# Kernel optimization log

Hardware: AMD Instinct MI355X
Metric: run time of the kernel (lower is better)

Reference implementation:

```python
import jax, jax.numpy as jnp
import numpy as np

T, N, F_IN = 5, 10000, 16
E = 160000
C = 32          # gat_hidden_dim (per head)
H0 = 2          # heads in layer 0 (concat) -> out 64
GRU = 64
OUT_H = 32


def setup_inputs() -> dict:
    key = jax.random.key(0)
    ks = jax.random.split(key, 24)
    s = 0.1
    inp = {
        "x_seq": jax.random.normal(ks[0], (T, N, F_IN), jnp.float32),
        "edge_index": jax.random.randint(ks[1], (2, E), 0, N, jnp.int32),
        # GAT layer 0: in 16 -> 2 heads x 32, concat -> 64
        "gat0_W": s * jax.random.normal(ks[2], (F_IN, H0 * C), jnp.float32),
        "gat0_asrc": s * jax.random.normal(ks[3], (H0, C), jnp.float32),
        "gat0_adst": s * jax.random.normal(ks[4], (H0, C), jnp.float32),
        "gat0_b": s * jax.random.normal(ks[5], (H0 * C,), jnp.float32),
        "res0_W": s * jax.random.normal(ks[6], (F_IN, H0 * C), jnp.float32),   # [in,out]
        # GAT layer 1: in 64 -> 1 head x 32, no concat -> 32
        "gat1_W": s * jax.random.normal(ks[7], (H0 * C, C), jnp.float32),
        "gat1_asrc": s * jax.random.normal(ks[8], (1, C), jnp.float32),
        "gat1_adst": s * jax.random.normal(ks[9], (1, C), jnp.float32),
        "gat1_b": s * jax.random.normal(ks[10], (C,), jnp.float32),
        "res1_W": s * jax.random.normal(ks[11], (H0 * C, C), jnp.float32),
        # GRU cells (torch GRUCell layout: W_i [3H,in], W_h [3H,H])
        "gru0_Wi": s * jax.random.normal(ks[12], (3 * GRU, C), jnp.float32),
        "gru0_Wh": s * jax.random.normal(ks[13], (3 * GRU, GRU), jnp.float32),
        "gru0_bi": s * jax.random.normal(ks[14], (3 * GRU,), jnp.float32),
        "gru0_bh": s * jax.random.normal(ks[15], (3 * GRU,), jnp.float32),
        "gru1_Wi": s * jax.random.normal(ks[16], (3 * GRU, GRU), jnp.float32),
        "gru1_Wh": s * jax.random.normal(ks[17], (3 * GRU, GRU), jnp.float32),
        "gru1_bi": s * jax.random.normal(ks[18], (3 * GRU,), jnp.float32),
        "gru1_bh": s * jax.random.normal(ks[19], (3 * GRU,), jnp.float32),
        # MLP head
        "fc1_W": s * jax.random.normal(ks[20], (GRU, OUT_H), jnp.float32),
        "fc1_b": s * jax.random.normal(ks[21], (OUT_H,), jnp.float32),
        "fc2_W": s * jax.random.normal(ks[22], (OUT_H, 1), jnp.float32),
        "fc2_b": s * jax.random.normal(ks[23], (1,), jnp.float32),
    }
    return inp


def _gat(x, src, dst, n, W, a_src, a_dst, b, heads, concat):
    ch = W.shape[1] // heads
    xw = (x @ W).reshape(n, heads, ch)                      # [N,H,C]
    al_s = (xw * a_src).sum(-1)                             # [N,H]
    al_d = (xw * a_dst).sum(-1)
    e = jax.nn.leaky_relu(al_s[src] + al_d[dst], 0.2)       # [Etot,H]
    m = jax.ops.segment_max(e, dst, num_segments=n)
    ex = jnp.exp(e - m[dst])
    den = jax.ops.segment_sum(ex, dst, num_segments=n)
    alpha = ex / (den[dst] + 1e-16)                         # scatter-softmax
    out = jax.ops.segment_sum(alpha[:, :, None] * xw[src], dst, num_segments=n)
    out = out.reshape(n, heads * ch) if concat else out.mean(axis=1)
    return out + b


def _gru(x, h, Wi, Wh, bi, bh):
    gi = x @ Wi.T + bi
    gh = h @ Wh.T + bh
    i_r, i_z, i_n = jnp.split(gi, 3, axis=-1)
    h_r, h_z, h_n = jnp.split(gh, 3, axis=-1)
    r = jax.nn.sigmoid(i_r + h_r)
    z = jax.nn.sigmoid(i_z + h_z)
    nn_ = jnp.tanh(i_n + r * h_n)
    return (1.0 - z) * nn_ + z * h


def reference(x_seq, edge_index,
              gat0_W, gat0_asrc, gat0_adst, gat0_b, res0_W,
              gat1_W, gat1_asrc, gat1_adst, gat1_b, res1_W,
              gru0_Wi, gru0_Wh, gru0_bi, gru0_bh,
              gru1_Wi, gru1_Wh, gru1_bi, gru1_bh,
              fc1_W, fc1_b, fc2_W, fc2_b):
    n = x_seq.shape[1]
    loops = jnp.arange(n, dtype=edge_index.dtype)
    src = jnp.concatenate([edge_index[0], loops])           # PyG adds self-loops
    dst = jnp.concatenate([edge_index[1], loops])

    def step(carry, x_t):
        h0, h1 = carry
        x1 = jax.nn.elu(_gat(x_t, src, dst, n, gat0_W, gat0_asrc, gat0_adst, gat0_b, 2, True)) + x_t @ res0_W
        x2 = jax.nn.elu(_gat(x1, src, dst, n, gat1_W, gat1_asrc, gat1_adst, gat1_b, 1, False)) + x1 @ res1_W
        h0 = _gru(x2, h0, gru0_Wi, gru0_Wh, gru0_bi, gru0_bh)
        h1 = _gru(h0, h1, gru1_Wi, gru1_Wh, gru1_bi, gru1_bh)
        return (h0, h1), None

    h0 = jnp.zeros((n, gru0_Wh.shape[1]), x_seq.dtype)
    h1 = jnp.zeros((n, gru1_Wh.shape[1]), x_seq.dtype)
    (h0, h1), _ = jax.lax.scan(step, (h0, h1), x_seq)
    h = jax.nn.relu(h1 @ fc1_W + fc1_b)
    return h @ fc2_W + fc2_b                                # [N,1]
```

## Files before the change

kernel.cpp:

```cpp
#include <hip/hip_runtime.h>
#include <hip/hip_bf16.h>
#include <math.h>

#define T_STEPS 5
#define NNODES  10000
#define NM      (T_STEPS * NNODES)
#define F_IN    16
#define NEDGES  160000
#define ETOT    (NEDGES + NNODES)

__global__ __launch_bounds__(256) void k_count(const int* __restrict__ ei, int* __restrict__ counts) {
    int idx = blockIdx.x * 256 + threadIdx.x;
    if (idx >= ETOT) return;
    int dst = (idx < NEDGES) ? ei[NEDGES + idx] : (idx - NEDGES);
    atomicAdd(&counts[dst], 1);
}

__global__ __launch_bounds__(1024) void k_scan(const int* __restrict__ counts, int* __restrict__ offs) {
    __shared__ int ssum[1024];
    int t = threadIdx.x;
    const int chunk = (NNODES + 1023) / 1024;
    int start = t * chunk, end = min(start + chunk, NNODES);
    int s = 0;
    for (int i = start; i < end; i++) s += counts[i];
    ssum[t] = s;
    __syncthreads();
    for (int off = 1; off < 1024; off <<= 1) {
        int v = (t >= off) ? ssum[t - off] : 0;
        __syncthreads();
        ssum[t] += v;
        __syncthreads();
    }
    int excl = (t == 0) ? 0 : ssum[t - 1];
    for (int i = start; i < end; i++) { offs[i] = excl; excl += counts[i]; }
    if (t == 1023) offs[NNODES] = ssum[1023];
}

__global__ __launch_bounds__(256) void k_fill(const int* __restrict__ ei, const int* __restrict__ offs,
                                              int* __restrict__ cursor, int* __restrict__ csr) {
    int idx = blockIdx.x * 256 + threadIdx.x;
    if (idx >= ETOT) return;
    int src, dst;
    if (idx < NEDGES) { src = ei[idx]; dst = ei[NEDGES + idx]; }
    else              { src = dst = idx - NEDGES; }
    int p = atomicAdd(&cursor[dst], 1);
    csr[offs[dst] + p] = src;
}

__global__ __launch_bounds__(256) void k_transpose(const float* __restrict__ Wi0, const float* __restrict__ Wh0,
                                                   const float* __restrict__ Wi1, const float* __restrict__ Wh1,
                                                   float* __restrict__ WiT0, float* __restrict__ WhT0,
                                                   float* __restrict__ WiT1, float* __restrict__ WhT1) {
    int idx = blockIdx.x * 256 + threadIdx.x;
    if (idx < 32 * 192) {
        int k = idx / 192, r = idx % 192;
        WiT0[idx] = Wi0[r * 32 + k];
        return;
    }
    idx -= 32 * 192;
    if (idx < 64 * 192) {
        int k = idx / 192, r = idx % 192;
        WhT0[idx] = Wh0[r * 64 + k];
        return;
    }
    idx -= 64 * 192;
    if (idx < 64 * 192) {
        int k = idx / 192, r = idx % 192;
        WiT1[idx] = Wi1[r * 64 + k];
        return;
    }
    idx -= 64 * 192;
    if (idx < 64 * 192) {
        int k = idx / 192, r = idx % 192;
        WhT1[idx] = Wh1[r * 64 + k];
    }
}

__global__ __launch_bounds__(256) void k_mm0_all(const float* __restrict__ x,
                                                 const float* __restrict__ W,
                                                 const float* __restrict__ Wres,
                                                 const float* __restrict__ asrc,
                                                 const float* __restrict__ adst,
                                                 float* __restrict__ xw, float* __restrict__ xres,
                                                 float* __restrict__ als, float* __restrict__ ald) {
    int wave = threadIdx.x >> 6, lane = threadIdx.x & 63;
    int m = blockIdx.x * 4 + wave;
    if (m >= NM) return;
    const float* xr = x + (size_t)m * F_IN;
    float xreg[F_IN];
#pragma unroll
    for (int k = 0; k < F_IN; k++) xreg[k] = xr[k];
    float acc = 0.f, accr = 0.f;
#pragma unroll
    for (int k = 0; k < F_IN; k++) {
        acc  += xreg[k] * W[k * 64 + lane];
        accr += xreg[k] * Wres[k * 64 + lane];
    }
    xw[(size_t)m * 64 + lane]   = acc;
    xres[(size_t)m * 64 + lane] = accr;
    float ps = acc * asrc[lane], pd = acc * adst[lane];
    for (int off = 16; off; off >>= 1) {
        ps += __shfl_down(ps, off, 32);
        pd += __shfl_down(pd, off, 32);
    }
    if ((lane & 31) == 0) {
        int h = lane >> 5;
        als[m * 2 + h] = ps;
        ald[m * 2 + h] = pd;
    }
}

__global__ __launch_bounds__(256) void k_gat0_all(const float* __restrict__ xw,
                                                  const float* __restrict__ xres,
                                                  const float* __restrict__ als,
                                                  const float* __restrict__ ald,
                                                  const int* __restrict__ offs, const int* __restrict__ csr,
                                                  const float* __restrict__ b,
                                                  const float* __restrict__ W1,
                                                  const float* __restrict__ Wres1,
                                                  const float* __restrict__ as1,
                                                  const float* __restrict__ ad1v,
                                                  float* __restrict__ xw1, float* __restrict__ xres1,
                                                  float* __restrict__ als1, float* __restrict__ ald1) {
    int wave = threadIdx.x >> 6, lane = threadIdx.x & 63;
    int m = blockIdx.x * 4 + wave;
    if (m >= NM) return;
    int t = m / NNODES;
    int node = m - t * NNODES;
    int base = t * NNODES;
    int beg = offs[node], end = offs[node + 1];
    int deg = end - beg;
    float ad0 = ald[m * 2 + 0], ad1 = ald[m * 2 + 1];
    float acc;
    if (deg <= 64) {
        int s = 0; float e0 = -INFINITY, e1 = -INFINITY;
        if (lane < deg) {
            s = base + csr[beg + lane];
            e0 = als[s * 2 + 0] + ad0; e0 = e0 > 0.f ? e0 : 0.2f * e0;
            e1 = als[s * 2 + 1] + ad1; e1 = e1 > 0.f ? e1 : 0.2f * e1;
        }
        float m0 = e0, m1 = e1;
        for (int o = 32; o; o >>= 1) {
            m0 = fmaxf(m0, __shfl_xor(m0, o));
            m1 = fmaxf(m1, __shfl_xor(m1, o));
        }
        float ex0 = (lane < deg) ? expf(e0 - m0) : 0.f;
        float ex1 = (lane < deg) ? expf(e1 - m1) : 0.f;
        float d0 = ex0, d1 = ex1;
        for (int o = 32; o; o >>= 1) {
            d0 += __shfl_xor(d0, o);
            d1 += __shfl_xor(d1, o);
        }
        ex0 *= 1.f / (d0 + 1e-16f);
        ex1 *= 1.f / (d1 + 1e-16f);
        float a0 = 0.f, a1 = 0.f, a2 = 0.f, a3 = 0.f;
        int i = 0;
        for (; i + 4 <= deg; i += 4) {
            int   s0 = __shfl(s, i),     s1 = __shfl(s, i + 1), s2 = __shfl(s, i + 2), s3 = __shfl(s, i + 3);
            float u0 = __shfl(ex0, i),   v0 = __shfl(ex1, i);
            float u1 = __shfl(ex0, i+1), v1 = __shfl(ex1, i+1);
            float u2 = __shfl(ex0, i+2), v2 = __shfl(ex1, i+2);
            float u3 = __shfl(ex0, i+3), v3 = __shfl(ex1, i+3);
            a0 += (lane < 32 ? u0 : v0) * xw[(size_t)s0 * 64 + lane];
            a1 += (lane < 32 ? u1 : v1) * xw[(size_t)s1 * 64 + lane];
            a2 += (lane < 32 ? u2 : v2) * xw[(size_t)s2 * 64 + lane];
            a3 += (lane < 32 ? u3 : v3) * xw[(size_t)s3 * 64 + lane];
        }
        for (; i < deg; i++) {
            int s0 = __shfl(s, i);
            float u = __shfl(ex0, i), v = __shfl(ex1, i);
            a0 += (lane < 32 ? u : v) * xw[(size_t)s0 * 64 + lane];
        }
        acc = (a0 + a1) + (a2 + a3);
    } else {
        float m0 = -INFINITY, m1 = -INFINITY;
        for (int i = beg + lane; i < end; i += 64) {
            int s = base + csr[i];
            float e0 = als[s * 2 + 0] + ad0; e0 = e0 > 0.f ? e0 : 0.2f * e0;
            float e1 = als[s * 2 + 1] + ad1; e1 = e1 > 0.f ? e1 : 0.2f * e1;
            m0 = fmaxf(m0, e0); m1 = fmaxf(m1, e1);
        }
        for (int o = 32; o; o >>= 1) {
            m0 = fmaxf(m0, __shfl_xor(m0, o));
            m1 = fmaxf(m1, __shfl_xor(m1, o));
        }
        float d0 = 0.f, d1 = 0.f;
        for (int i = beg + lane; i < end; i += 64) {
            int s = base + csr[i];
            float e0 = als[s * 2 + 0] + ad0; e0 = e0 > 0.f ? e0 : 0.2f * e0;
            float e1 = als[s * 2 + 1] + ad1; e1 = e1 > 0.f ? e1 : 0.2f * e1;
            d0 += expf(e0 - m0); d1 += expf(e1 - m1);
        }
        for (int o = 32; o; o >>= 1) { d0 += __shfl_xor(d0, o); d1 += __shfl_xor(d1, o); }
        float inv0 = 1.f / (d0 + 1e-16f), inv1 = 1.f / (d1 + 1e-16f);
        acc = 0.f;
        for (int i = beg; i < end; i++) {
            int s = base + csr[i];
            float e, wgt;
            if (lane < 32) { e = als[s * 2 + 0] + ad0; e = e > 0.f ? e : 0.2f * e; wgt = expf(e - m0) * inv0; }
            else           { e = als[s * 2 + 1] + ad1; e = e > 0.f ? e : 0.2f * e; wgt = expf(e - m1) * inv1; }
            acc += wgt * xw[(size_t)s * 64 + lane];
        }
    }
    float x1v = acc + b[lane];
    x1v = x1v > 0.f ? x1v : expm1f(x1v);
    x1v += xres[(size_t)m * 64 + lane];
    int j = lane & 31;
    const float* Wp = (lane < 32) ? W1 : Wres1;
    float pacc = 0.f;
#pragma unroll
    for (int k = 0; k < 64; k++) {
        float xv = __shfl(x1v, k);
        pacc += xv * Wp[k * 32 + j];
    }
    if (lane < 32) xw1[(size_t)m * 32 + j]   = pacc;
    else           xres1[(size_t)m * 32 + j] = pacc;
    float ps = (lane < 32) ? pacc * as1[j]  : 0.f;
    float pd = (lane < 32) ? pacc * ad1v[j] : 0.f;
    for (int o = 16; o; o >>= 1) {
        ps += __shfl_down(ps, o, 32);
        pd += __shfl_down(pd, o, 32);
    }
    if (lane == 0) { als1[m] = ps; ald1[m] = pd; }
}

__global__ __launch_bounds__(256) void k_gat1_all(const float* __restrict__ xw1,
                                                  const float* __restrict__ xres1,
                                                  const float* __restrict__ als1,
                                                  const float* __restrict__ ald1,
                                                  const int* __restrict__ offs, const int* __restrict__ csr,
                                                  const float* __restrict__ b,
                                                  float* __restrict__ x2) {
    int wave = threadIdx.x >> 6, lane = threadIdx.x & 63;
    int m = blockIdx.x * 4 + wave;
    if (m >= NM) return;
    int t = m / NNODES;
    int node = m - t * NNODES;
    int base = t * NNODES;
    int beg = offs[node], end = offs[node + 1];
    int deg = end - beg;
    float adv = ald1[m];
    int ch = lane & 31, half = lane >> 5;
    float aggr;
    if (deg <= 64) {
        int s = 0; float e = -INFINITY;
        if (lane < deg) {
            s = base + csr[beg + lane];
            e = als1[s] + adv; e = e > 0.f ? e : 0.2f * e;
        }
        float mx = e;
        for (int o = 32; o; o >>= 1) mx = fmaxf(mx, __shfl_xor(mx, o));
        float ex = (lane < deg) ? expf(e - mx) : 0.f;
        float d = ex;
        for (int o = 32; o; o >>= 1) d += __shfl_xor(d, o);
        ex *= 1.f / (d + 1e-16f);
        float acc = 0.f;
        for (int i = 0; i < deg; i += 2) {
            int i2 = (i + 1 < deg) ? i + 1 : i;
            int   sa = __shfl(s, i),  sb = __shfl(s, i2);
            float wa = __shfl(ex, i), wb = __shfl(ex, i2);
            if (i + 1 >= deg) wb = 0.f;
            int   sm = half ? sb : sa;
            float wm = half ? wb : wa;
            acc += wm * xw1[(size_t)sm * 32 + ch];
        }
        acc += __shfl_xor(acc, 32);
        aggr = acc;
    } else {
        float mx = -INFINITY;
        for (int i = beg + lane; i < end; i += 64) {
            float e = als1[base + csr[i]] + adv; e = e > 0.f ? e : 0.2f * e;
            mx = fmaxf(mx, e);
        }
        for (int o = 32; o; o >>= 1) mx = fmaxf(mx, __shfl_xor(mx, o));
        float d = 0.f;
        for (int i = beg + lane; i < end; i += 64) {
            float e = als1[base + csr[i]] + adv; e = e > 0.f ? e : 0.2f * e;
            d += expf(e - mx);
        }
        for (int o = 32; o; o >>= 1) d += __shfl_xor(d, o);
        float inv = 1.f / (d + 1e-16f);
        float acc = 0.f;
        for (int i = beg; i < end; i++) {
            int s = base + csr[i];
            float e = als1[s] + adv; e = e > 0.f ? e : 0.2f * e;
            float wgt = expf(e - mx) * inv;
            acc += wgt * xw1[(size_t)s * 32 + ch];
        }
        aggr = acc;
    }
    if (lane < 32) {
        float v = aggr + b[ch];
        v = v > 0.f ? v : expm1f(v);
        x2[(size_t)m * 32 + ch] = v + xres1[(size_t)m * 32 + ch];
    }
}

__global__ __launch_bounds__(256) void k_gruhead(const float* __restrict__ x2,
                                                 const float* __restrict__ WiT0,
                                                 const float* __restrict__ WhT0,
                                                 const float* __restrict__ WiT1,
                                                 const float* __restrict__ WhT1,
                                                 const float* __restrict__ bi0, const float* __restrict__ bh0,
                                                 const float* __restrict__ bi1, const float* __restrict__ bh1,
                                                 const float* __restrict__ fc1W,
                                                 const float* __restrict__ fc1b,
                                                 const float* __restrict__ fc2W,
                                                 const float* __restrict__ fc2b,
                                                 float* __restrict__ out) {
    int wave = threadIdx.x >> 6, lane = threadIdx.x & 63;
    int node0 = (blockIdx.x * 4 + wave) * 2;

    float bir0 = bi0[lane], biz0 = bi0[64 + lane], bin0 = bi0[128 + lane];
    float bhr0 = bh0[lane], bhz0 = bh0[64 + lane], bhn0 = bh0[128 + lane];
    float bir1 = bi1[lane], biz1 = bi1[64 + lane], bin1 = bi1[128 + lane];
    float bhr1 = bh1[lane], bhz1 = bh1[64 + lane], bhn1 = bh1[128 + lane];

    float h0v0 = 0.f, h0v1 = 0.f, h1v0 = 0.f, h1v1 = 0.f;

    for (int t = 0; t < T_STEPS; t++) {
        float x2v = x2[((size_t)t * NNODES + node0) * 32 + lane];

        float gr0 = bir0, gz0 = biz0, gn0 = bin0, gr1 = bir0, gz1 = biz0, gn1 = bin0;
        float hr0 = bhr0, hz0 = bhz0, hn0 = bhn0, hr1 = bhr0, hz1 = bhz0, hn1 = bhn0;
#pragma unroll 8
        for (int k = 0; k < 32; k++) {
            float wr = WiT0[k * 192 + lane];
            float wz = WiT0[k * 192 + 64 + lane];
            float wn = WiT0[k * 192 + 128 + lane];
            float xa = __shfl(x2v, k);
            float xb = __shfl(x2v, 32 + k);
            gr0 += xa * wr; gz0 += xa * wz; gn0 += xa * wn;
            gr1 += xb * wr; gz1 += xb * wz; gn1 += xb * wn;
        }
#pragma unroll 8
        for (int k = 0; k < 64; k++) {
            float wr = WhT0[k * 192 + lane];
            float wz = WhT0[k * 192 + 64 + lane];
            float wn = WhT0[k * 192 + 128 + lane];
            float ha = __shfl(h0v0, k);
            float hb = __shfl(h0v1, k);
            hr0 += ha * wr; hz0 += ha * wz; hn0 += ha * wn;
            hr1 += hb * wr; hz1 += hb * wz; hn1 += hb * wn;
        }
        {
            float r0 = 1.f / (1.f + expf(-(gr0 + hr0)));
            float z0 = 1.f / (1.f + expf(-(gz0 + hz0)));
            float n0 = tanhf(gn0 + r0 * hn0);
            h0v0 = (1.f - z0) * n0 + z0 * h0v0;
            float r1 = 1.f / (1.f + expf(-(gr1 + hr1)));
            float z1 = 1.f / (1.f + expf(-(gz1 + hz1)));
            float n1 = tanhf(gn1 + r1 * hn1);
            h0v1 = (1.f - z1) * n1 + z1 * h0v1;
        }
        gr0 = bir1; gz0 = biz1; gn0 = bin1; gr1 = bir1; gz1 = biz1; gn1 = bin1;
        hr0 = bhr1; hz0 = bhz1; hn0 = bhn1; hr1 = bhr1; hz1 = bhz1; hn1 = bhn1;
#pragma unroll 4
        for (int k = 0; k < 64; k++) {
            float wir = WiT1[k * 192 + lane];
            float wiz = WiT1[k * 192 + 64 + lane];
            float win = WiT1[k * 192 + 128 + lane];
            float xa = __shfl(h0v0, k);
            float xb = __shfl(h0v1, k);
            gr0 += xa * wir; gz0 += xa * wiz; gn0 += xa * win;
            gr1 += xb * wir; gz1 += xb * wiz; gn1 += xb * win;
            float whr = WhT1[k * 192 + lane];
            float whz = WhT1[k * 192 + 64 + lane];
            float whn = WhT1[k * 192 + 128 + lane];
            float ha = __shfl(h1v0, k);
            float hb = __shfl(h1v1, k);
            hr0 += ha * whr; hz0 += ha * whz; hn0 += ha * whn;
            hr1 += hb * whr; hz1 += hb * whz; hn1 += hb * whn;
        }
        {
            float r0 = 1.f / (1.f + expf(-(gr0 + hr0)));
            float z0 = 1.f / (1.f + expf(-(gz0 + hz0)));
            float n0 = tanhf(gn0 + r0 * hn0);
            h1v0 = (1.f - z0) * n0 + z0 * h1v0;
            float r1 = 1.f / (1.f + expf(-(gr1 + hr1)));
            float z1 = 1.f / (1.f + expf(-(gz1 + hz1)));
            float n1 = tanhf(gn1 + r1 * hn1);
            h1v1 = (1.f - z1) * n1 + z1 * h1v1;
        }
    }

    int j = lane & 31, half = lane >> 5;
    float a = fc1b[j];
#pragma unroll
    for (int k = 0; k < 64; k++) {
        float h_a = __shfl(h1v0, k);
        float h_b = __shfl(h1v1, k);
        a += (half ? h_b : h_a) * fc1W[k * 32 + j];
    }
    a = fmaxf(a, 0.f);
    float v = a * fc2W[j];
    for (int o = 16; o; o >>= 1) v += __shfl_down(v, o, 32);
    if ((lane & 31) == 0) out[node0 + half] = v + fc2b[0];
}

extern "C" void kernel_launch(void* const* d_in, const int* in_sizes, int n_in,
                              void* d_out, int out_size, void* d_ws, size_t ws_size,
                              hipStream_t stream) {
    const float* x_seq   = (const float*)d_in[0];
    const int*   ei      = (const int*)d_in[1];
    const float* gat0_W  = (const float*)d_in[2];
    const float* gat0_as = (const float*)d_in[3];
    const float* gat0_ad = (const float*)d_in[4];
    const float* gat0_b  = (const float*)d_in[5];
    const float* res0_W  = (const float*)d_in[6];
    const float* gat1_W  = (const float*)d_in[7];
    const float* gat1_as = (const float*)d_in[8];
    const float* gat1_ad = (const float*)d_in[9];
    const float* gat1_b  = (const float*)d_in[10];
    const float* res1_W  = (const float*)d_in[11];
    const float* gru0_Wi = (const float*)d_in[12];
    const float* gru0_Wh = (const float*)d_in[13];
    const float* gru0_bi = (const float*)d_in[14];
    const float* gru0_bh = (const float*)d_in[15];
    const float* gru1_Wi = (const float*)d_in[16];
    const float* gru1_Wh = (const float*)d_in[17];
    const float* gru1_bi = (const float*)d_in[18];
    const float* gru1_bh = (const float*)d_in[19];
    const float* fc1_W   = (const float*)d_in[20];
    const float* fc1_b   = (const float*)d_in[21];
    const float* fc2_W   = (const float*)d_in[22];
    const float* fc2_b   = (const float*)d_in[23];
    float* out = (float*)d_out;

    char* w = (char*)d_ws;
    size_t off = 0;
    auto take = [&](size_t bytes) { size_t r = off; off += (bytes + 255) & ~(size_t)255; return r; };
    const size_t N = NNODES, M = NM;
    int*   counts = (int*)(w + take(N * 4));
    int*   cursor = (int*)(w + take(N * 4));
    int*   offs   = (int*)(w + take((N + 1) * 4));
    int*   csr    = (int*)(w + take((size_t)ETOT * 4));
    float* xw0    = (float*)(w + take(M * 64 * 4));
    float* xres0  = (float*)(w + take(M * 64 * 4));
    float* als0   = (float*)(w + take(M * 2 * 4));
    float* ald0   = (float*)(w + take(M * 2 * 4));
    float* xw1    = (float*)(w + take(M * 32 * 4));
    float* xres1  = (float*)(w + take(M * 32 * 4));
    float* als1   = (float*)(w + take(M * 4));
    float* ald1   = (float*)(w + take(M * 4));
    float* x2     = (float*)(w + take(M * 32 * 4));
    float* wiT0   = (float*)(w + take(32 * 192 * 4));
    float* whT0   = (float*)(w + take(64 * 192 * 4));
    float* wiT1   = (float*)(w + take(64 * 192 * 4));
    float* whT1   = (float*)(w + take(64 * 192 * 4));

    hipMemsetAsync(counts, 0, N * 4, stream);
    hipMemsetAsync(cursor, 0, N * 4, stream);
    const int egrid = (ETOT + 255) / 256;
    k_count<<<egrid, 256, 0, stream>>>(ei, counts);
    k_scan<<<1, 1024, 0, stream>>>(counts, offs);
    k_fill<<<egrid, 256, 0, stream>>>(ei, offs, cursor, csr);
    const int ttot = 32 * 192 + 3 * 64 * 192;
    k_transpose<<<(ttot + 255) / 256, 256, 0, stream>>>(gru0_Wi, gru0_Wh, gru1_Wi, gru1_Wh,
                                                        wiT0, whT0, wiT1, whT1);

    const int mgrid = (NM + 3) / 4;
    k_mm0_all<<<mgrid, 256, 0, stream>>>(x_seq, gat0_W, res0_W, gat0_as, gat0_ad, xw0, xres0, als0, ald0);
    k_gat0_all<<<mgrid, 256, 0, stream>>>(xw0, xres0, als0, ald0, offs, csr, gat0_b,
                                          gat1_W, res1_W, gat1_as, gat1_ad,
                                          xw1, xres1, als1, ald1);
    k_gat1_all<<<mgrid, 256, 0, stream>>>(xw1, xres1, als1, ald1, offs, csr, gat1_b, x2);

    const int ggrid = NNODES / 8;
    k_gruhead<<<ggrid, 256, 0, stream>>>(x2, wiT0, whT0, wiT1, whT1,
                                         gru0_bi, gru0_bh, gru1_bi, gru1_bh,
                                         fc1_W, fc1_b, fc2_W, fc2_b, out);
}
```

Before: 444.9 us.

## Process four nodes per wave in GRU head and use readlane broadcasts

The GRU/MLP head kernel now handles four nodes per wavefront instead of two, so each weight load is reused across more nodes. The r and z gate biases are pre-summed and the input and hidden matmuls are merged into shared accumulators. Lane broadcasts switch from __shfl (LDS-based permute) to the readlane builtin, which returns a wave-uniform scalar, and this also applies in the gat0 projection. The trade-offs are higher register pressure and half as many waves in the GRU kernel, which lowers occupancy.

```diff
diff --git a/kernel.cpp b/kernel.cpp
--- a/kernel.cpp
+++ b/kernel.cpp
@@ -8,6 +8,9 @@
 #define F_IN    16
 #define NEDGES  160000
 #define ETOT    (NEDGES + NNODES)
+#define GNPW    4
+
+#define RL(v, k) __int_as_float(__builtin_amdgcn_readlane(__float_as_int(v), (k)))
 
 __global__ __launch_bounds__(256) void k_count(const int* __restrict__ ei, int* __restrict__ counts) {
     int idx = blockIdx.x * 256 + threadIdx.x;
@@ -210,7 +213,7 @@
     float pacc = 0.f;
 #pragma unroll
     for (int k = 0; k < 64; k++) {
-        float xv = __shfl(x1v, k);
+        float xv = RL(x1v, k);
         pacc += xv * Wp[k * 32 + j];
     }
     if (lane < 32) xw1[(size_t)m * 32 + j]   = pacc;
@@ -309,93 +312,101 @@
                                                  const float* __restrict__ fc2b,
                                                  float* __restrict__ out) {
     int wave = threadIdx.x >> 6, lane = threadIdx.x & 63;
-    int node0 = (blockIdx.x * 4 + wave) * 2;
-
-    float bir0 = bi0[lane], biz0 = bi0[64 + lane], bin0 = bi0[128 + lane];
-    float bhr0 = bh0[lane], bhz0 = bh0[64 + lane], bhn0 = bh0[128 + lane];
-    float bir1 = bi1[lane], biz1 = bi1[64 + lane], bin1 = bi1[128 + lane];
-    float bhr1 = bh1[lane], bhz1 = bh1[64 + lane], bhn1 = bh1[128 + lane];
-
-    float h0v0 = 0.f, h0v1 = 0.f, h1v0 = 0.f, h1v1 = 0.f;
+    int node0 = (blockIdx.x * 4 + wave) * GNPW;
+
+    float bir0 = bi0[lane] + bh0[lane];
+    float biz0 = bi0[64 + lane] + bh0[64 + lane];
+    float bin0 = bi0[128 + lane], bhn0 = bh0[128 + lane];
+    float bir1 = bi1[lane] + bh1[lane];
+    float biz1 = bi1[64 + lane] + bh1[64 + lane];
+    float bin1 = bi1[128 + lane], bhn1 = bh1[128 + lane];
+
+    float h0[GNPW] = {0.f, 0.f, 0.f, 0.f};
+    float h1[GNPW] = {0.f, 0.f, 0.f, 0.f};
 
     for (int t = 0; t < T_STEPS; t++) {
-        float x2v = x2[((size_t)t * NNODES + node0) * 32 + lane];
-
-        float gr0 = bir0, gz0 = biz0, gn0 = bin0, gr1 = bir0, gz1 = biz0, gn1 = bin0;
-        float hr0 = bhr0, hz0 = bhz0, hn0 = bhn0, hr1 = bhr0, hz1 = bhz0, hn1 = bhn0;
+        float xa = x2[((size_t)t * NNODES + node0) * 32 + lane];
+        float xb = x2[((size_t)t * NNODES + node0) * 32 + 64 + lane];
+
+        float gr[GNPW], gz[GNPW], gin[GNPW], ghn[GNPW];
+#pragma unroll
+        for (int n = 0; n < GNPW; n++) { gr[n] = bir0; gz[n] = biz0; gin[n] = bin0; ghn[n] = bhn0; }
 #pragma unroll 8
         for (int k = 0; k < 32; k++) {
             float wr = WiT0[k * 192 + lane];
             float wz = WiT0[k * 192 + 64 + lane];
             float wn = WiT0[k * 192 + 128 + lane];
-            float xa = __shfl(x2v, k);
-            float xb = __shfl(x2v, 32 + k);
-            gr0 += xa * wr; gz0 += xa * wz; gn0 += xa * wn;
-            gr1 += xb * wr; gz1 += xb * wz; gn1 += xb * wn;
-        }
-#pragma unroll 8
+            float xv[GNPW];
+            xv[0] = RL(xa, k); xv[1] = RL(xa, 32 + k);
+            xv[2] = RL(xb, k); xv[3] = RL(xb, 32 + k);
+#pragma unroll
+            for (int n = 0; n < GNPW; n++) {
+                gr[n] += xv[n] * wr; gz[n] += xv[n] * wz; gin[n] += xv[n] * wn;
+            }
+        }
+#pragma unroll 4
         for (int k = 0; k < 64; k++) {
             float wr = WhT0[k * 192 + lane];
             float wz = WhT0[k * 192 + 64 + lane];
             float wn = WhT0[k * 192 + 128 + lane];
-            float ha = __shfl(h0v0, k);
-            float hb = __shfl(h0v1, k);
-            hr0 += ha * wr; hz0 += ha * wz; hn0 += ha * wn;
-            hr1 += hb * wr; hz1 += hb * wz; hn1 += hb * wn;
-        }
-        {
-            float r0 = 1.f / (1.f + expf(-(gr0 + hr0)));
-            float z0 = 1.f / (1.f + expf(-(gz0 + hz0)));
-            float n0 = tanhf(gn0 + r0 * hn0);
-            h0v0 = (1.f - z0) * n0 + z0 * h0v0;
-            float r1 = 1.f / (1.f + expf(-(gr1 + hr1)));
-            float z1 = 1.f / (1.f + expf(-(gz1 + hz1)));
-            float n1 = tanhf(gn1 + r1 * hn1);
-            h0v1 = (1.f - z1) * n1 + z1 * h0v1;
-        }
-        gr0 = bir1; gz0 = biz1; gn0 = bin1; gr1 = bir1; gz1 = biz1; gn1 = bin1;
-        hr0 = bhr1; hz0 = bhz1; hn0 = bhn1; hr1 = bhr1; hz1 = bhz1; hn1 = bhn1;
+#pragma unroll
+            for (int n = 0; n < GNPW; n++) {
+                float hv = RL(h0[n], k);
+                gr[n] += hv * wr; gz[n] += hv * wz; ghn[n] += hv * wn;
+            }
+        }
+#pragma unroll
+        for (int n = 0; n < GNPW; n++) {
+            float r = 1.f / (1.f + expf(-gr[n]));
+            float z = 1.f / (1.f + expf(-gz[n]));
+            float nn = tanhf(gin[n] + r * ghn[n]);
+            h0[n] = (1.f - z) * nn + z * h0[n];
+        }
+
+#pragma unroll
+        for (int n = 0; n < GNPW; n++) { gr[n] = bir1; gz[n] = biz1; gin[n] = bin1; ghn[n] = bhn1; }
 #pragma unroll 4
         for (int k = 0; k < 64; k++) {
             float wir = WiT1[k * 192 + lane];
             float wiz = WiT1[k * 192 + 64 + lane];
             float win = WiT1[k * 192 + 128 + lane];
-            float xa = __shfl(h0v0, k);
-            float xb = __shfl(h0v1, k);
-            gr0 += xa * wir; gz0 += xa * wiz; gn0 += xa * win;
-            gr1 += xb * wir; gz1 += xb * wiz; gn1 += xb * win;
             float whr = WhT1[k * 192 + lane];
             float whz = WhT1[k * 192 + 64 + lane];
             float whn = WhT1[k * 192 + 128 + lane];
-            float ha = __shfl(h1v0, k);
-            float hb = __shfl(h1v1, k);
-            hr0 += ha * whr; hz0 += ha * whz; hn0 += ha * whn;
-            hr1 += hb * whr; hz1 += hb * whz; hn1 += hb * whn;
-        }
-        {
-            float r0 = 1.f / (1.f + expf(-(gr0 + hr0)));
-            float z0 = 1.f / (1.f + expf(-(gz0 + hz0)));
-            float n0 = tanhf(gn0 + r0 * hn0);
-            h1v0 = (1.f - z0) * n0 + z0 * h1v0;
-            float r1 = 1.f / (1.f + expf(-(gr1 + hr1)));
-            float z1 = 1.f / (1.f + expf(-(gz1 + hz1)));
-            float n1 = tanhf(gn1 + r1 * hn1);
-            h1v1 = (1.f - z1) * n1 + z1 * h1v1;
+#pragma unroll
+            for (int n = 0; n < GNPW; n++) {
+                float xv = RL(h0[n], k);
+                float hv = RL(h1[n], k);
+                gr[n] += xv * wir + hv * whr;
+                gz[n] += xv * wiz + hv * whz;
+                gin[n] += xv * win;
+                ghn[n] += hv * whn;
+            }
+        }
+#pragma unroll
+        for (int n = 0; n < GNPW; n++) {
+            float r = 1.f / (1.f + expf(-gr[n]));
+            float z = 1.f / (1.f + expf(-gz[n]));
+            float nn = tanhf(gin[n] + r * ghn[n]);
+            h1[n] = (1.f - z) * nn + z * h1[n];
         }
     }
 
     int j = lane & 31, half = lane >> 5;
-    float a = fc1b[j];
-#pragma unroll
-    for (int k = 0; k < 64; k++) {
-        float h_a = __shfl(h1v0, k);
-        float h_b = __shfl(h1v1, k);
-        a += (half ? h_b : h_a) * fc1W[k * 32 + j];
-    }
-    a = fmaxf(a, 0.f);
-    float v = a * fc2W[j];
-    for (int o = 16; o; o >>= 1) v += __shfl_down(v, o, 32);
-    if ((lane & 31) == 0) out[node0 + half] = v + fc2b[0];
+#pragma unroll
+    for (int p = 0; p < 2; p++) {
+        float a = fc1b[j];
+#pragma unroll
+        for (int k = 0; k < 64; k++) {
+            float he = RL(h1[2 * p], k);
+            float ho = RL(h1[2 * p + 1], k);
+            a += (half ? ho : he) * fc1W[k * 32 + j];
+        }
+        a = fmaxf(a, 0.f);
+        float v = a * fc2W[j];
+        for (int o = 16; o; o >>= 1) v += __shfl_down(v, o, 32);
+        if ((lane & 31) == 0) out[node0 + 2 * p + half] = v + fc2b[0];
+    }
 }
 
 extern "C" void kernel_launch(void* const* d_in, const int* in_sizes, int n_in,
@@ -466,7 +477,7 @@
                                           xw1, xres1, als1, ald1);
     k_gat1_all<<<mgrid, 256, 0, stream>>>(xw1, xres1, als1, ald1, offs, csr, gat1_b, x2);
 
-    const int ggrid = NNODES / 8;
+    const int ggrid = NNODES / (4 * GNPW);
     k_gruhead<<<ggrid, 256, 0, stream>>>(x2, wiT0, whT0, wiT1, whT1,
                                          gru0_bi, gru0_bh, gru1_bi, gru1_bh,
                                          fc1_W, fc1_b, fc2_W, fc2_b, out);
```

New measurement: 417.5 us. -6.1%, faster.
